# Kernel tuning notes

Hardware: AMD Instinct MI355X
Metric: run time of the kernel (lower is better)

The kernel has to match this reference:

```python
import jax, jax.numpy as jnp
import numpy as np

EMBED = 1024
HEAD = 64

def setup_inputs() -> dict:
    key = jax.random.key(0)
    k1, k2, k3, k4 = jax.random.split(key, 4)
    # Torch Linear weight layout: [out_features, in_features]; xavier_uniform init
    bound = float(np.sqrt(6.0 / (EMBED + HEAD)))
    embeddings = jax.random.normal(k1, (4, 4096, EMBED), dtype=jnp.float32)
    W_Q = jax.random.uniform(k2, (HEAD, EMBED), dtype=jnp.float32, minval=-bound, maxval=bound)
    W_K = jax.random.uniform(k3, (HEAD, EMBED), dtype=jnp.float32, minval=-bound, maxval=bound)
    W_V = jax.random.uniform(k4, (HEAD, EMBED), dtype=jnp.float32, minval=-bound, maxval=bound)
    return {"embeddings": embeddings, "W_Q": W_Q, "W_K": W_K, "W_V": W_V}

def reference(embeddings, W_Q, W_K, W_V):
    # embeddings: [B, S, E]; weights: [H, E] (torch Linear layout, y = x @ W.T)
    B, S, E = embeddings.shape
    H = W_Q.shape[0]
    Q = jnp.einsum('bse,he->bsh', embeddings, W_Q)
    K = jnp.einsum('bse,he->bsh', embeddings, W_K)
    V = jnp.einsum('bse,he->bsh', embeddings, W_V)
    scale = 1.0 / jnp.sqrt(jnp.float32(H))
    scores = jnp.einsum('bqh,bkh->bqk', Q, K) * scale  # [B, S, S]
    causal = jnp.tril(jnp.ones((S, S), dtype=bool))
    scores = jnp.where(causal, scores, -jnp.inf)
    attn = jax.nn.softmax(scores, axis=-1)
    # dropout (p=0.1) is identity at inference; omitted for determinism
    return jnp.einsum('bqk,bkh->bqh', attn, V)  # [B, S, H]
```

## Files before the change

### kernel.cpp

```cpp
#include <hip/hip_runtime.h>
#include <hip/hip_bf16.h>

#define EMBED 1024
#define SEQ   4096
#define NBATCH 4
#define HD    64
#define CHUNK 16

typedef __attribute__((ext_vector_type(8))) short s16x8;
typedef __attribute__((ext_vector_type(4))) float f32x4;

__device__ __forceinline__ short f2bf(float f) {
    unsigned u = __builtin_bit_cast(unsigned, f);
    u += 0x7fffu + ((u >> 16) & 1u);
    return (short)(u >> 16);
}
__device__ __forceinline__ float bf2f(short h) {
    unsigned u = ((unsigned)(unsigned short)h) << 16;
    return __builtin_bit_cast(float, u);
}

typedef const unsigned int __attribute__((address_space(1)))* gbl_ptr_t;
typedef unsigned int __attribute__((address_space(3)))* lds_ptr_t;
__device__ __forceinline__ void async16(const void* g, void* l) {
    __builtin_amdgcn_global_load_lds((gbl_ptr_t)g, (lds_ptr_t)l, 16, 0, 0);
}

__global__ __launch_bounds__(256) void prep_w(
    const float* __restrict__ wq, const float* __restrict__ wk,
    const float* __restrict__ wv, short* __restrict__ Wb)
{
    int idx = blockIdx.x * 256 + threadIdx.x;
    int e = idx * 8;
    int row = e >> 10, col = e & 1023;
    const float* src = (row < 64) ? (wq + (size_t)row * EMBED)
                     : (row < 128) ? (wk + (size_t)(row - 64) * EMBED)
                                   : (wv + (size_t)(row - 128) * EMBED);
    float sc = (row < 64) ? 0.125f : 1.0f;
    float4 f0 = *(const float4*)(src + col);
    float4 f1 = *(const float4*)(src + col + 4);
    s16x8 v = { f2bf(f0.x*sc), f2bf(f0.y*sc), f2bf(f0.z*sc), f2bf(f0.w*sc),
                f2bf(f1.x*sc), f2bf(f1.y*sc), f2bf(f1.z*sc), f2bf(f1.w*sc) };
    *(s16x8*)&Wb[e] = v;
}

__global__ __launch_bounds__(256) void proj_qkv(
    const float* __restrict__ emb, const short* __restrict__ Wb,
    short* __restrict__ Qb, short* __restrict__ Kb, short* __restrict__ Vt)
{
    __shared__ short Alds[2][32 * 64];
    __shared__ short Blds[2][192 * 64];

    const int tid  = threadIdx.x;
    const int lane = tid & 63;
    const int w    = tid >> 6;
    const int wr   = w & 1;
    const int wc   = w >> 1;
    const int row0 = blockIdx.x * 32;

    const int sr   = tid >> 3;
    const int sg   = tid & 7;
    const int srow = lane >> 3;
    const int sblk = lane & 7;

    f32x4 acc[6];
#pragma unroll
    for (int i = 0; i < 6; ++i) acc[i] = f32x4{0.f, 0.f, 0.f, 0.f};

    auto stageB = [&](int buf, int t) {
        const int k0 = t * 64;
#pragma unroll
        for (int i = 0; i < 6; ++i) {
            int r = w * 48 + i * 8 + srow;
            async16(Wb + (size_t)r * EMBED + k0 + ((sblk ^ (r & 7)) * 8),
                    &Blds[buf][(w * 48 + i * 8) * 64]);
        }
    };

    {
        const float* asrc = emb + (size_t)(row0 + sr) * EMBED + sg * 8;
        float4 f0 = *(const float4*)asrc;
        float4 f1 = *(const float4*)(asrc + 4);
        s16x8 v = { f2bf(f0.x), f2bf(f0.y), f2bf(f0.z), f2bf(f0.w),
                    f2bf(f1.x), f2bf(f1.y), f2bf(f1.z), f2bf(f1.w) };
        *(s16x8*)&Alds[0][sr * 64 + ((sg ^ (sr & 7)) * 8)] = v;
        stageB(0, 0);
    }
    __syncthreads();

    int cur = 0;
    const int ar = wr * 16 + (lane & 15);
    const int ag = lane >> 4;

    for (int t = 0; t < 16; ++t) {
        float4 f0n, f1n;
        const bool more = (t + 1 < 16);
        if (more) {
            const float* asrc = emb + (size_t)(row0 + sr) * EMBED + (t + 1) * 64 + sg * 8;
            f0n = *(const float4*)asrc;
            f1n = *(const float4*)(asrc + 4);
            stageB(cur ^ 1, t + 1);
        }
        s16x8 a0 = *(const s16x8*)&Alds[cur][ar * 64 + (((ag    ) ^ (ar & 7)) * 8)];
        s16x8 a1 = *(const s16x8*)&Alds[cur][ar * 64 + (((ag + 4) ^ (ar & 7)) * 8)];
#pragma unroll
        for (int n = 0; n < 6; ++n) {
            int br = wc * 96 + n * 16 + (lane & 15);
            s16x8 b0 = *(const s16x8*)&Blds[cur][br * 64 + (((ag    ) ^ (br & 7)) * 8)];
            s16x8 b1 = *(const s16x8*)&Blds[cur][br * 64 + (((ag + 4) ^ (br & 7)) * 8)];
            acc[n] = __builtin_amdgcn_mfma_f32_16x16x32_bf16(a0, b0, acc[n], 0, 0, 0);
            acc[n] = __builtin_amdgcn_mfma_f32_16x16x32_bf16(a1, b1, acc[n], 0, 0, 0);
        }
        if (more) {
            s16x8 v = { f2bf(f0n.x), f2bf(f0n.y), f2bf(f0n.z), f2bf(f0n.w),
                        f2bf(f1n.x), f2bf(f1n.y), f2bf(f1n.z), f2bf(f1n.w) };
            *(s16x8*)&Alds[cur ^ 1][sr * 64 + ((sg ^ (sr & 7)) * 8)] = v;
        }
        __syncthreads();
        cur ^= 1;
    }

    const int rbase = row0 + wr * 16 + ((lane >> 4) * 4);
    const int cl = lane & 15;
#pragma unroll
    for (int n = 0; n < 6; ++n) {
        int col = wc * 96 + n * 16 + cl;
        int mat = col >> 6;
        int c = col & 63;
#pragma unroll
        for (int r = 0; r < 4; ++r) {
            int row = rbase + r;
            int b = row >> 12, s = row & 4095;
            short v = f2bf(acc[n][r]);
            if (mat == 0)       Qb[((size_t)b * SEQ + s) * HD + c] = v;
            else if (mat == 1)  Kb[((size_t)b * SEQ + s) * HD + c] = v;
            else                Vt[((size_t)b * HD + c) * SEQ + s] = v;
        }
    }
}

__global__ __launch_bounds__(256) void attn_fwd(
    const short* __restrict__ Qb, const short* __restrict__ Kb,
    const short* __restrict__ Vt, float* __restrict__ Op, float* __restrict__ Ml)
{
    const int jq = blockIdx.x;
    const int b  = blockIdx.y;
    const int p  = blockIdx.z;
    const int ntiles = jq + 1;
    const int t0 = p * CHUNK;
    if (t0 >= ntiles) return;
    const int t1 = min(t0 + CHUNK, ntiles);

    __shared__ short Qlds[64 * 64];
    __shared__ short Klds[2][64 * 64];
    __shared__ short Vlds[2][64 * 64];
    __shared__ short Plds[64 * 64];

    const int tid  = threadIdx.x;
    const int lane = tid & 63;
    const int w    = tid >> 6;
    const int q0   = jq * 64;

    const short* Qbase  = Qb + ((size_t)b * SEQ + q0) * HD;
    const short* Kbase0 = Kb + (size_t)b * SEQ * HD;
    const short* Vbase0 = Vt + (size_t)b * HD * SEQ;

    const int srow = lane >> 3;
    const int sblk = lane & 7;

    auto stageKV = [&](int buf, int t) {
        const int kv0 = t * 64;
#pragma unroll
        for (int i = 0; i < 2; ++i) {
            int r = w * 16 + i * 8 + srow;
            async16(Kbase0 + (size_t)(kv0 + r) * HD + ((sblk ^ (r & 7)) * 8),
                    &Klds[buf][(w * 16 + i * 8) * 64]);
            async16(Vbase0 + (size_t)r * SEQ + kv0 + ((sblk ^ (r & 7)) * 8),
                    &Vlds[buf][(w * 16 + i * 8) * 64]);
        }
    };

#pragma unroll
    for (int i = 0; i < 2; ++i) {
        int r = w * 16 + i * 8 + srow;
        async16(Qbase + (size_t)r * HD + ((sblk ^ (r & 7)) * 8),
                &Qlds[(w * 16 + i * 8) * 64]);
    }
    stageKV(0, t0);
    __syncthreads();

    const int qrow = w * 16 + (lane & 15);
    const int ag = lane >> 4;
    s16x8 qa0 = *(const s16x8*)&Qlds[qrow * 64 + (((ag    ) ^ (qrow & 7)) * 8)];
    s16x8 qa1 = *(const s16x8*)&Qlds[qrow * 64 + (((ag + 4) ^ (qrow & 7)) * 8)];

    f32x4 o[4];
#pragma unroll
    for (int n = 0; n < 4; ++n) o[n] = f32x4{0.f, 0.f, 0.f, 0.f};
    float m[4], l[4];
#pragma unroll
    for (int r = 0; r < 4; ++r) { m[r] = -INFINITY; l[r] = 0.f; }

    int cur = 0;
    for (int t = t0; t < t1; ++t) {
        if (t + 1 < t1) stageKV(cur ^ 1, t + 1);

        const int kv0 = t * 64;
        f32x4 s[4];
#pragma unroll
        for (int n = 0; n < 4; ++n) {
            int kr = n * 16 + (lane & 15);
            s16x8 b0 = *(const s16x8*)&Klds[cur][kr * 64 + (((ag    ) ^ (kr & 7)) * 8)];
            s16x8 b1 = *(const s16x8*)&Klds[cur][kr * 64 + (((ag + 4) ^ (kr & 7)) * 8)];
            s[n] = __builtin_amdgcn_mfma_f32_16x16x32_bf16(qa0, b0, f32x4{0.f,0.f,0.f,0.f}, 0, 0, 0);
            s[n] = __builtin_amdgcn_mfma_f32_16x16x32_bf16(qa1, b1, s[n], 0, 0, 0);
        }

        if (t == jq) {
            int qg = q0 + w * 16 + ((lane >> 4) * 4);
#pragma unroll
            for (int n = 0; n < 4; ++n) {
                int kvg = kv0 + n * 16 + (lane & 15);
#pragma unroll
                for (int r = 0; r < 4; ++r)
                    if (kvg > qg + r) s[n][r] = -INFINITY;
            }
        }

        float mt[4];
#pragma unroll
        for (int r = 0; r < 4; ++r)
            mt[r] = fmaxf(fmaxf(s[0][r], s[1][r]), fmaxf(s[2][r], s[3][r]));
#pragma unroll
        for (int d = 1; d < 16; d <<= 1) {
#pragma unroll
            for (int r = 0; r < 4; ++r)
                mt[r] = fmaxf(mt[r], __shfl_xor(mt[r], d, 64));
        }
        float fac[4];
#pragma unroll
        for (int r = 0; r < 4; ++r) {
            float mn = fmaxf(m[r], mt[r]);
            fac[r] = __expf(m[r] - mn);
            m[r] = mn;
        }
        float rs[4] = {0.f, 0.f, 0.f, 0.f};
#pragma unroll
        for (int n = 0; n < 4; ++n) {
#pragma unroll
            for (int r = 0; r < 4; ++r) {
                float pv = __expf(s[n][r] - m[r]);
                short pb = f2bf(pv);
                rs[r] += bf2f(pb);
                int q  = w * 16 + ((lane >> 4) * 4) + r;
                int kv = n * 16 + (lane & 15);
                Plds[q * 64 + (((kv >> 3) ^ (q & 7)) * 8) + (kv & 7)] = pb;
            }
        }
#pragma unroll
        for (int d = 1; d < 16; d <<= 1) {
#pragma unroll
            for (int r = 0; r < 4; ++r)
                rs[r] += __shfl_xor(rs[r], d, 64);
        }
#pragma unroll
        for (int r = 0; r < 4; ++r) l[r] = l[r] * fac[r] + rs[r];
#pragma unroll
        for (int n = 0; n < 4; ++n)
#pragma unroll
            for (int r = 0; r < 4; ++r) o[n][r] *= fac[r];

#pragma unroll
        for (int kk = 0; kk < 2; ++kk) {
            int pr = w * 16 + (lane & 15);
            s16x8 pa = *(const s16x8*)&Plds[pr * 64 + (((ag + kk * 4) ^ (pr & 7)) * 8)];
#pragma unroll
            for (int n = 0; n < 4; ++n) {
                int vr = n * 16 + (lane & 15);
                s16x8 vb = *(const s16x8*)&Vlds[cur][vr * 64 + (((ag + kk * 4) ^ (vr & 7)) * 8)];
                o[n] = __builtin_amdgcn_mfma_f32_16x16x32_bf16(pa, vb, o[n], 0, 0, 0);
            }
        }
        __syncthreads();
        cur ^= 1;
    }

    float* opbase = Op + (((size_t)b * 64 + jq) * 4 + p) * 64 * 64;
    float* mlbase = Ml + (((size_t)b * 64 + jq) * 4 + p) * 64 * 2;
#pragma unroll
    for (int r = 0; r < 4; ++r) {
        int ql = w * 16 + ((lane >> 4) * 4) + r;
        if ((lane & 15) == 0) {
            mlbase[ql * 2]     = m[r];
            mlbase[ql * 2 + 1] = l[r];
        }
#pragma unroll
        for (int n = 0; n < 4; ++n)
            opbase[(size_t)ql * 64 + n * 16 + (lane & 15)] = o[n][r];
    }
}

__global__ __launch_bounds__(256) void attn_combine(
    const float* __restrict__ Op, const float* __restrict__ Ml,
    float* __restrict__ out)
{
    const int jq = blockIdx.x;
    const int b  = blockIdx.y;
    const int nP = (jq >> 4) + 1;
    const int tid = threadIdx.x;
    const int row = tid >> 2;
    const int c0  = (tid & 3) * 16;
    const size_t pb = ((size_t)b * 64 + jq) * 4;

    float mv[4], lv[4], wt[4];
    float mstar = -INFINITY;
#pragma unroll
    for (int p = 0; p < 4; ++p) if (p < nP) {
        mv[p] = Ml[(pb + p) * 128 + row * 2];
        lv[p] = Ml[(pb + p) * 128 + row * 2 + 1];
        mstar = fmaxf(mstar, mv[p]);
    }
    float L = 0.f;
#pragma unroll
    for (int p = 0; p < 4; ++p) if (p < nP) {
        wt[p] = __expf(mv[p] - mstar);
        L += lv[p] * wt[p];
    }
    float inv = 1.0f / L;

    float acc[16];
#pragma unroll
    for (int k = 0; k < 16; ++k) acc[k] = 0.f;
#pragma unroll
    for (int p = 0; p < 4; ++p) if (p < nP) {
        const float* src = &Op[((pb + p) * 64 + row) * 64 + c0];
#pragma unroll
        for (int k = 0; k < 16; ++k) acc[k] += src[k] * wt[p];
    }
    float* dst = out + ((size_t)b * SEQ + jq * 64 + row) * HD + c0;
#pragma unroll
    for (int k = 0; k < 16; ++k) dst[k] = acc[k] * inv;
}

extern "C" void kernel_launch(void* const* d_in, const int* in_sizes, int n_in,
                              void* d_out, int out_size, void* d_ws, size_t ws_size,
                              hipStream_t stream)
{
    (void)in_sizes; (void)n_in; (void)out_size; (void)ws_size;
    const float* emb = (const float*)d_in[0];
    const float* wq  = (const float*)d_in[1];
    const float* wk  = (const float*)d_in[2];
    const float* wv  = (const float*)d_in[3];
    float* out = (float*)d_out;

    short* Wb = (short*)d_ws;
    short* Qb = Wb + 192 * 1024;
    short* Kb = Qb + (size_t)NBATCH * SEQ * HD;
    short* Vt = Kb + (size_t)NBATCH * SEQ * HD;
    float* Op = (float*)(Vt + (size_t)NBATCH * SEQ * HD);
    float* Ml = Op + (size_t)NBATCH * 64 * 4 * 64 * 64;

    hipLaunchKernelGGL(prep_w, dim3(96), dim3(256), 0, stream, wq, wk, wv, Wb);
    hipLaunchKernelGGL(proj_qkv, dim3(512), dim3(256), 0, stream, emb, Wb, Qb, Kb, Vt);
    hipLaunchKernelGGL(attn_fwd, dim3(64, NBATCH, 4), dim3(256), 0, stream,
                       Qb, Kb, Vt, Op, Ml);
    hipLaunchKernelGGL(attn_combine, dim3(64, NBATCH), dim3(256), 0, stream,
                       Op, Ml, out);
}
```

Baseline: 166.5 us.

## Rewrite attention loop register-resident with transposed S, finer KV split

The attention kernel drops its shared-memory staging of Q, K, V and P. It loads K and V fragments straight from global memory into registers and computes S transposed (K as the A operand), so each lane owns a single query row. P is rearranged across lanes with shuffles instead of a round trip through LDS, and the loop needs no barriers. The KV split doubles from 4 to 8 chunks of 8 tiles to spread causal work more evenly, and the combine kernel is updated for the new partial layout. The projection kernel prefetches embeddings two steps ahead. The risks are uncoalesced direct global loads, higher register pressure, and more partial-result traffic in the combine step.

```diff
diff --git a/kernel.cpp b/kernel.cpp
--- a/kernel.cpp
+++ b/kernel.cpp
@@ -5,10 +5,12 @@
 #define SEQ   4096
 #define NBATCH 4
 #define HD    64
-#define CHUNK 16
+#define CH    8
+#define NP    8
 
 typedef __attribute__((ext_vector_type(8))) short s16x8;
 typedef __attribute__((ext_vector_type(4))) float f32x4;
+typedef __attribute__((ext_vector_type(4))) unsigned int u32x4;
 
 __device__ __forceinline__ short f2bf(float f) {
     unsigned u = __builtin_bit_cast(unsigned, f);
@@ -76,31 +78,33 @@
                     &Blds[buf][(w * 48 + i * 8) * 64]);
         }
     };
-
-    {
-        const float* asrc = emb + (size_t)(row0 + sr) * EMBED + sg * 8;
-        float4 f0 = *(const float4*)asrc;
-        float4 f1 = *(const float4*)(asrc + 4);
+    const float* abase = emb + (size_t)(row0 + sr) * EMBED + sg * 8;
+    auto writeA = [&](int buf, float4 f0, float4 f1) {
         s16x8 v = { f2bf(f0.x), f2bf(f0.y), f2bf(f0.z), f2bf(f0.w),
                     f2bf(f1.x), f2bf(f1.y), f2bf(f1.z), f2bf(f1.w) };
-        *(s16x8*)&Alds[0][sr * 64 + ((sg ^ (sr & 7)) * 8)] = v;
-        stageB(0, 0);
-    }
+        *(s16x8*)&Alds[buf][sr * 64 + ((sg ^ (sr & 7)) * 8)] = v;
+    };
+
+    float4 f0a = *(const float4*)(abase);
+    float4 f1a = *(const float4*)(abase + 4);
+    stageB(0, 0);
+    writeA(0, f0a, f1a);
+    f0a = *(const float4*)(abase + 64);
+    f1a = *(const float4*)(abase + 68);
     __syncthreads();
 
     int cur = 0;
     const int ar = wr * 16 + (lane & 15);
     const int ag = lane >> 4;
+    float4 f0b = f0a, f1b = f1a;
 
     for (int t = 0; t < 16; ++t) {
-        float4 f0n, f1n;
-        const bool more = (t + 1 < 16);
-        if (more) {
-            const float* asrc = emb + (size_t)(row0 + sr) * EMBED + (t + 1) * 64 + sg * 8;
-            f0n = *(const float4*)asrc;
-            f1n = *(const float4*)(asrc + 4);
-            stageB(cur ^ 1, t + 1);
-        }
+        if (t < 14) {
+            f0b = *(const float4*)(abase + (size_t)(t + 2) * 64);
+            f1b = *(const float4*)(abase + (size_t)(t + 2) * 64 + 4);
+        }
+        stageB(cur ^ 1, t + 1 < 16 ? t + 1 : 15);
+
         s16x8 a0 = *(const s16x8*)&Alds[cur][ar * 64 + (((ag    ) ^ (ar & 7)) * 8)];
         s16x8 a1 = *(const s16x8*)&Alds[cur][ar * 64 + (((ag + 4) ^ (ar & 7)) * 8)];
 #pragma unroll
@@ -111,12 +115,9 @@
             acc[n] = __builtin_amdgcn_mfma_f32_16x16x32_bf16(a0, b0, acc[n], 0, 0, 0);
             acc[n] = __builtin_amdgcn_mfma_f32_16x16x32_bf16(a1, b1, acc[n], 0, 0, 0);
         }
-        if (more) {
-            s16x8 v = { f2bf(f0n.x), f2bf(f0n.y), f2bf(f0n.z), f2bf(f0n.w),
-                        f2bf(f1n.x), f2bf(f1n.y), f2bf(f1n.z), f2bf(f1n.w) };
-            *(s16x8*)&Alds[cur ^ 1][sr * 64 + ((sg ^ (sr & 7)) * 8)] = v;
-        }
+        writeA(cur ^ 1, f0a, f1a);
         __syncthreads();
+        f0a = f0b; f1a = f1b;
         cur ^= 1;
     }
 
@@ -146,157 +147,136 @@
     const int jq = blockIdx.x;
     const int b  = blockIdx.y;
     const int p  = blockIdx.z;
-    const int ntiles = jq + 1;
-    const int t0 = p * CHUNK;
-    if (t0 >= ntiles) return;
-    const int t1 = min(t0 + CHUNK, ntiles);
-
-    __shared__ short Qlds[64 * 64];
-    __shared__ short Klds[2][64 * 64];
-    __shared__ short Vlds[2][64 * 64];
-    __shared__ short Plds[64 * 64];
+    const int t0 = p * CH;
+    if (t0 > jq) return;
+    const int t1 = min(t0 + CH, jq + 1);
 
     const int tid  = threadIdx.x;
     const int lane = tid & 63;
     const int w    = tid >> 6;
-    const int q0   = jq * 64;
-
-    const short* Qbase  = Qb + ((size_t)b * SEQ + q0) * HD;
-    const short* Kbase0 = Kb + (size_t)b * SEQ * HD;
-    const short* Vbase0 = Vt + (size_t)b * HD * SEQ;
-
-    const int srow = lane >> 3;
-    const int sblk = lane & 7;
-
-    auto stageKV = [&](int buf, int t) {
-        const int kv0 = t * 64;
-#pragma unroll
-        for (int i = 0; i < 2; ++i) {
-            int r = w * 16 + i * 8 + srow;
-            async16(Kbase0 + (size_t)(kv0 + r) * HD + ((sblk ^ (r & 7)) * 8),
-                    &Klds[buf][(w * 16 + i * 8) * 64]);
-            async16(Vbase0 + (size_t)r * SEQ + kv0 + ((sblk ^ (r & 7)) * 8),
-                    &Vlds[buf][(w * 16 + i * 8) * 64]);
+    const int l15  = lane & 15;
+    const int g    = lane >> 4;
+    const int q0w  = jq * 64 + w * 16;
+
+    const short* Kb_b = Kb + (size_t)b * SEQ * HD;
+    const short* Vt_b = Vt + (size_t)b * HD * SEQ;
+
+    const short* qp = Qb + ((size_t)b * SEQ + q0w + l15) * HD + g * 8;
+    s16x8 qb0 = *(const s16x8*)qp;
+    s16x8 qb1 = *(const s16x8*)(qp + 32);
+
+    f32x4 o[4];
+#pragma unroll
+    for (int n = 0; n < 4; ++n) o[n] = f32x4{0.f, 0.f, 0.f, 0.f};
+    float m = -INFINITY, l = 0.f;
+
+    s16x8 ka0[4], ka1[4];
+    auto loadK = [&](int t) {
+        const short* kp = Kb_b + ((size_t)t * 64 + l15) * HD + g * 8;
+#pragma unroll
+        for (int n = 0; n < 4; ++n) {
+            ka0[n] = *(const s16x8*)(kp + n * 16 * HD);
+            ka1[n] = *(const s16x8*)(kp + n * 16 * HD + 32);
         }
     };
-
-#pragma unroll
-    for (int i = 0; i < 2; ++i) {
-        int r = w * 16 + i * 8 + srow;
-        async16(Qbase + (size_t)r * HD + ((sblk ^ (r & 7)) * 8),
-                &Qlds[(w * 16 + i * 8) * 64]);
-    }
-    stageKV(0, t0);
-    __syncthreads();
-
-    const int qrow = w * 16 + (lane & 15);
-    const int ag = lane >> 4;
-    s16x8 qa0 = *(const s16x8*)&Qlds[qrow * 64 + (((ag    ) ^ (qrow & 7)) * 8)];
-    s16x8 qa1 = *(const s16x8*)&Qlds[qrow * 64 + (((ag + 4) ^ (qrow & 7)) * 8)];
-
-    f32x4 o[4];
-#pragma unroll
-    for (int n = 0; n < 4; ++n) o[n] = f32x4{0.f, 0.f, 0.f, 0.f};
-    float m[4], l[4];
-#pragma unroll
-    for (int r = 0; r < 4; ++r) { m[r] = -INFINITY; l[r] = 0.f; }
-
-    int cur = 0;
+    loadK(t0);
+
+    const int f1l = (2 * (g & 1) + (g >> 1)) * 16 + l15;
+    const int f2l = (2 * (g & 1) + 1 - (g >> 1)) * 16 + l15;
+    const bool podd = (g & 1) != 0;
+    const bool hbit = (g >> 1) != 0;
+
     for (int t = t0; t < t1; ++t) {
-        if (t + 1 < t1) stageKV(cur ^ 1, t + 1);
-
-        const int kv0 = t * 64;
-        f32x4 s[4];
+        f32x4 st[4];
 #pragma unroll
         for (int n = 0; n < 4; ++n) {
-            int kr = n * 16 + (lane & 15);
-            s16x8 b0 = *(const s16x8*)&Klds[cur][kr * 64 + (((ag    ) ^ (kr & 7)) * 8)];
-            s16x8 b1 = *(const s16x8*)&Klds[cur][kr * 64 + (((ag + 4) ^ (kr & 7)) * 8)];
-            s[n] = __builtin_amdgcn_mfma_f32_16x16x32_bf16(qa0, b0, f32x4{0.f,0.f,0.f,0.f}, 0, 0, 0);
-            s[n] = __builtin_amdgcn_mfma_f32_16x16x32_bf16(qa1, b1, s[n], 0, 0, 0);
-        }
+            st[n] = __builtin_amdgcn_mfma_f32_16x16x32_bf16(ka0[n], qb0, f32x4{0.f,0.f,0.f,0.f}, 0, 0, 0);
+            st[n] = __builtin_amdgcn_mfma_f32_16x16x32_bf16(ka1[n], qb1, st[n], 0, 0, 0);
+        }
+        loadK(t + 1 < t1 ? t + 1 : t);
+
+        s16x8 va[4][2];
+#pragma unroll
+        for (int n = 0; n < 4; ++n)
+#pragma unroll
+            for (int kk = 0; kk < 2; ++kk)
+                va[n][kk] = *(const s16x8*)(Vt_b + (size_t)(n * 16 + l15) * SEQ
+                                            + (size_t)t * 64 + kk * 32 + g * 8);
 
         if (t == jq) {
-            int qg = q0 + w * 16 + ((lane >> 4) * 4);
-#pragma unroll
-            for (int n = 0; n < 4; ++n) {
-                int kvg = kv0 + n * 16 + (lane & 15);
-#pragma unroll
-                for (int r = 0; r < 4; ++r)
-                    if (kvg > qg + r) s[n][r] = -INFINITY;
-            }
-        }
-
-        float mt[4];
+#pragma unroll
+            for (int n = 0; n < 4; ++n)
+#pragma unroll
+                for (int r = 0; r < 4; ++r) {
+                    int kvg = t * 64 + n * 16 + g * 4 + r;
+                    if (kvg > q0w + l15) st[n][r] = -INFINITY;
+                }
+        }
+
+        float mt = fmaxf(fmaxf(st[0][0], st[0][1]), fmaxf(st[0][2], st[0][3]));
+#pragma unroll
+        for (int n = 1; n < 4; ++n)
+            mt = fmaxf(mt, fmaxf(fmaxf(st[n][0], st[n][1]), fmaxf(st[n][2], st[n][3])));
+        mt = fmaxf(mt, __shfl_xor(mt, 16, 64));
+        mt = fmaxf(mt, __shfl_xor(mt, 32, 64));
+
+        float mn  = fmaxf(m, mt);
+        float fac = __expf(m - mn);
+        m = mn;
+
+        float rs = 0.f;
+        unsigned pk[4][2];
+#pragma unroll
+        for (int n = 0; n < 4; ++n) {
+            unsigned u0 = (unsigned)(unsigned short)f2bf(__expf(st[n][0] - m));
+            unsigned u1 = (unsigned)(unsigned short)f2bf(__expf(st[n][1] - m));
+            unsigned u2 = (unsigned)(unsigned short)f2bf(__expf(st[n][2] - m));
+            unsigned u3 = (unsigned)(unsigned short)f2bf(__expf(st[n][3] - m));
+            pk[n][0] = u0 | (u1 << 16);
+            pk[n][1] = u2 | (u3 << 16);
+            rs += bf2f((short)u0) + bf2f((short)u1) + bf2f((short)u2) + bf2f((short)u3);
+        }
+        rs += __shfl_xor(rs, 16, 64);
+        rs += __shfl_xor(rs, 32, 64);
+        l = l * fac + rs;
+#pragma unroll
+        for (int n = 0; n < 4; ++n)
+#pragma unroll
+            for (int r = 0; r < 4; ++r) o[n][r] *= fac;
+
+#pragma unroll
+        for (int kk = 0; kk < 2; ++kk) {
+            unsigned e00 = podd ? pk[2 * kk + 1][0] : pk[2 * kk][0];
+            unsigned e01 = podd ? pk[2 * kk + 1][1] : pk[2 * kk][1];
+            unsigned e10 = podd ? pk[2 * kk][0]     : pk[2 * kk + 1][0];
+            unsigned e11 = podd ? pk[2 * kk][1]     : pk[2 * kk + 1][1];
+            unsigned x0 = (unsigned)__shfl((int)e00, f1l, 64);
+            unsigned x1 = (unsigned)__shfl((int)e01, f1l, 64);
+            unsigned y0 = (unsigned)__shfl((int)e10, f2l, 64);
+            unsigned y1 = (unsigned)__shfl((int)e11, f2l, 64);
+            unsigned w0 = hbit ? y0 : x0;
+            unsigned w1 = hbit ? y1 : x1;
+            unsigned w2 = hbit ? x0 : y0;
+            unsigned w3 = hbit ? x1 : y1;
+            u32x4 uu = { w0, w1, w2, w3 };
+            s16x8 pb = __builtin_bit_cast(s16x8, uu);
+#pragma unroll
+            for (int n = 0; n < 4; ++n)
+                o[n] = __builtin_amdgcn_mfma_f32_16x16x32_bf16(va[n][kk], pb, o[n], 0, 0, 0);
+        }
+    }
+
+    const size_t pidx = ((size_t)b * 64 + jq) * NP + p;
+    float* opb = Op + pidx * 4096;
+#pragma unroll
+    for (int n = 0; n < 4; ++n)
 #pragma unroll
         for (int r = 0; r < 4; ++r)
-            mt[r] = fmaxf(fmaxf(s[0][r], s[1][r]), fmaxf(s[2][r], s[3][r]));
-#pragma unroll
-        for (int d = 1; d < 16; d <<= 1) {
-#pragma unroll
-            for (int r = 0; r < 4; ++r)
-                mt[r] = fmaxf(mt[r], __shfl_xor(mt[r], d, 64));
-        }
-        float fac[4];
-#pragma unroll
-        for (int r = 0; r < 4; ++r) {
-            float mn = fmaxf(m[r], mt[r]);
-            fac[r] = __expf(m[r] - mn);
-            m[r] = mn;
-        }
-        float rs[4] = {0.f, 0.f, 0.f, 0.f};
-#pragma unroll
-        for (int n = 0; n < 4; ++n) {
-#pragma unroll
-            for (int r = 0; r < 4; ++r) {
-                float pv = __expf(s[n][r] - m[r]);
-                short pb = f2bf(pv);
-                rs[r] += bf2f(pb);
-                int q  = w * 16 + ((lane >> 4) * 4) + r;
-                int kv = n * 16 + (lane & 15);
-                Plds[q * 64 + (((kv >> 3) ^ (q & 7)) * 8) + (kv & 7)] = pb;
-            }
-        }
-#pragma unroll
-        for (int d = 1; d < 16; d <<= 1) {
-#pragma unroll
-            for (int r = 0; r < 4; ++r)
-                rs[r] += __shfl_xor(rs[r], d, 64);
-        }
-#pragma unroll
-        for (int r = 0; r < 4; ++r) l[r] = l[r] * fac[r] + rs[r];
-#pragma unroll
-        for (int n = 0; n < 4; ++n)
-#pragma unroll
-            for (int r = 0; r < 4; ++r) o[n][r] *= fac[r];
-
-#pragma unroll
-        for (int kk = 0; kk < 2; ++kk) {
-            int pr = w * 16 + (lane & 15);
-            s16x8 pa = *(const s16x8*)&Plds[pr * 64 + (((ag + kk * 4) ^ (pr & 7)) * 8)];
-#pragma unroll
-            for (int n = 0; n < 4; ++n) {
-                int vr = n * 16 + (lane & 15);
-                s16x8 vb = *(const s16x8*)&Vlds[cur][vr * 64 + (((ag + kk * 4) ^ (vr & 7)) * 8)];
-                o[n] = __builtin_amdgcn_mfma_f32_16x16x32_bf16(pa, vb, o[n], 0, 0, 0);
-            }
-        }
-        __syncthreads();
-        cur ^= 1;
-    }
-
-    float* opbase = Op + (((size_t)b * 64 + jq) * 4 + p) * 64 * 64;
-    float* mlbase = Ml + (((size_t)b * 64 + jq) * 4 + p) * 64 * 2;
-#pragma unroll
-    for (int r = 0; r < 4; ++r) {
-        int ql = w * 16 + ((lane >> 4) * 4) + r;
-        if ((lane & 15) == 0) {
-            mlbase[ql * 2]     = m[r];
-            mlbase[ql * 2 + 1] = l[r];
-        }
-#pragma unroll
-        for (int n = 0; n < 4; ++n)
-            opbase[(size_t)ql * 64 + n * 16 + (lane & 15)] = o[n][r];
+            opb[(n * 16 + g * 4 + r) * 64 + w * 16 + l15] = o[n][r];
+    if (lane < 16) {
+        float* mlb = Ml + pidx * 128;
+        mlb[w * 16 + l15]      = m;
+        mlb[64 + w * 16 + l15] = l;
     }
 }
 
@@ -306,23 +286,23 @@
 {
     const int jq = blockIdx.x;
     const int b  = blockIdx.y;
-    const int nP = (jq >> 4) + 1;
+    const int nP = (jq >> 3) + 1;
     const int tid = threadIdx.x;
-    const int row = tid >> 2;
-    const int c0  = (tid & 3) * 16;
-    const size_t pb = ((size_t)b * 64 + jq) * 4;
-
-    float mv[4], lv[4], wt[4];
+    const int q  = tid & 63;
+    const int dc = tid >> 6;
+    const size_t pb = ((size_t)b * 64 + jq) * NP;
+
+    float mv[NP], lv[NP], wt[NP];
     float mstar = -INFINITY;
 #pragma unroll
-    for (int p = 0; p < 4; ++p) if (p < nP) {
-        mv[p] = Ml[(pb + p) * 128 + row * 2];
-        lv[p] = Ml[(pb + p) * 128 + row * 2 + 1];
+    for (int p = 0; p < NP; ++p) if (p < nP) {
+        mv[p] = Ml[(pb + p) * 128 + q];
+        lv[p] = Ml[(pb + p) * 128 + 64 + q];
         mstar = fmaxf(mstar, mv[p]);
     }
     float L = 0.f;
 #pragma unroll
-    for (int p = 0; p < 4; ++p) if (p < nP) {
+    for (int p = 0; p < NP; ++p) if (p < nP) {
         wt[p] = __expf(mv[p] - mstar);
         L += lv[p] * wt[p];
     }
@@ -332,12 +312,12 @@
 #pragma unroll
     for (int k = 0; k < 16; ++k) acc[k] = 0.f;
 #pragma unroll
-    for (int p = 0; p < 4; ++p) if (p < nP) {
-        const float* src = &Op[((pb + p) * 64 + row) * 64 + c0];
-#pragma unroll
-        for (int k = 0; k < 16; ++k) acc[k] += src[k] * wt[p];
-    }
-    float* dst = out + ((size_t)b * SEQ + jq * 64 + row) * HD + c0;
+    for (int p = 0; p < NP; ++p) if (p < nP) {
+        const float* src = Op + (pb + p) * 4096 + (size_t)dc * 16 * 64 + q;
+#pragma unroll
+        for (int k = 0; k < 16; ++k) acc[k] += src[k * 64] * wt[p];
+    }
+    float* dst = out + ((size_t)b * SEQ + jq * 64 + q) * HD + dc * 16;
 #pragma unroll
     for (int k = 0; k < 16; ++k) dst[k] = acc[k] * inv;
 }
@@ -358,11 +338,11 @@
     short* Kb = Qb + (size_t)NBATCH * SEQ * HD;
     short* Vt = Kb + (size_t)NBATCH * SEQ * HD;
     float* Op = (float*)(Vt + (size_t)NBATCH * SEQ * HD);
-    float* Ml = Op + (size_t)NBATCH * 64 * 4 * 64 * 64;
+    float* Ml = Op + (size_t)NBATCH * 64 * NP * 64 * 64;
 
     hipLaunchKernelGGL(prep_w, dim3(96), dim3(256), 0, stream, wq, wk, wv, Wb);
     hipLaunchKernelGGL(proj_qkv, dim3(512), dim3(256), 0, stream, emb, Wb, Qb, Kb, Vt);
-    hipLaunchKernelGGL(attn_fwd, dim3(64, NBATCH, 4), dim3(256), 0, stream,
+    hipLaunchKernelGGL(attn_fwd, dim3(64, NBATCH, NP), dim3(256), 0, stream,
                        Qb, Kb, Vt, Op, Ml);
     hipLaunchKernelGGL(attn_combine, dim3(64, NBATCH), dim3(256), 0, stream,
                        Op, Ml, out);
```

New measurement: 217.3 us. +30.5%, slower.
